# Performance work log

Measured on AMD Instinct MI355X. Metric: run time of the kernel, lower is better.

## Reference

```python
import jax, jax.numpy as jnp
import numpy as np

N_EMBED = 384

def setup_inputs() -> dict:
    key = jax.random.key(0)
    kx, kq, kk, kv = jax.random.split(key, 4)
    B, T, C = 512, 256, N_EMBED
    H = 64
    scale = 1.0 / np.sqrt(C)  # param init scale, keep activations sane
    x = jax.random.normal(kx, (B, T, C), dtype=jnp.float32)
    Wq = jax.random.normal(kq, (C, H), dtype=jnp.float32) * scale
    Wk = jax.random.normal(kk, (C, H), dtype=jnp.float32) * scale
    Wv = jax.random.normal(kv, (C, H), dtype=jnp.float32) * scale
    return {"x": x, "Wq": Wq, "Wk": Wk, "Wv": Wv}

def reference(x, Wq, Wk, Wv):
    B, T, C = x.shape
    q = jnp.einsum('btc,ch->bth', x, Wq)
    k = jnp.einsum('btc,ch->bth', x, Wk)
    v = jnp.einsum('btc,ch->bth', x, Wv)
    # NOTE: original scales by C**-0.5 with C = n_embed (384), not head_size.
    wei = jnp.einsum('bth,bsh->bts', q, k) * (C ** -0.5)  # [B,T,T]
    causal = jnp.tril(jnp.ones((T, T), dtype=bool))
    wei = jnp.where(causal, wei, -jnp.inf)
    wei = jax.nn.softmax(wei, axis=-1)
    out = jnp.einsum('bts,bsh->bth', wei, v)  # [B,T,H]
    return out
```

## Files before the change

kernel.cpp:

```cpp
#include <hip/hip_runtime.h>
#include <hip/hip_bf16.h>


constexpr int BSZ  = 512;
constexpr int TT   = 256;
constexpr int CDIM = 384;
constexpr int HDIM = 64;
constexpr int NQKV = 192;
constexpr float SCALE = 0.051031036307982884f;
constexpr int BTST = 392;

typedef __attribute__((ext_vector_type(8))) short bf16x8;
typedef __attribute__((ext_vector_type(4))) float f32x4;

__device__ inline unsigned short f2bf(float f) {
    __hip_bfloat16 h = __float2bfloat16(f);
    return *(unsigned short*)&h;
}
__device__ inline bf16x8 pack8(float4 a, float4 b) {
    unsigned short p[8] = { f2bf(a.x), f2bf(a.y), f2bf(a.z), f2bf(a.w),
                            f2bf(b.x), f2bf(b.y), f2bf(b.z), f2bf(b.w) };
    return *(bf16x8*)p;
}
__device__ inline unsigned cvtpk(float lo, float hi) {
    unsigned r;
    asm volatile("v_cvt_pk_bf16_f32 %0, %1, %2" : "=v"(r) : "v"(lo), "v"(hi));
    return r;
}
#define PLSWAP32(a, b) asm volatile("v_permlane32_swap_b32 %0, %1" : "+v"(a), "+v"(b))
#define PLSWAP16(a, b) asm volatile("v_permlane16_swap_b32 %0, %1" : "+v"(a), "+v"(b))

__global__ __launch_bounds__(256) void prep_bt(
    const float* __restrict__ Wq, const float* __restrict__ Wk,
    const float* __restrict__ Wv, unsigned short* __restrict__ bt)
{
    int idx = blockIdx.x * 256 + threadIdx.x;
    if (idx >= NQKV * CDIM) return;
    int n = idx / CDIM, k = idx - n * CDIM;
    const float* W = (n < 64) ? Wq : (n < 128) ? Wk : Wv;
    bt[idx] = f2bf(W[(size_t)k * HDIM + (n & 63)]);
}

__global__ __launch_bounds__(1024) void fused(
    const float* __restrict__ x, const unsigned short* __restrict__ bt,
    float* __restrict__ out)
{
    __shared__ __align__(16) unsigned short smem[NQKV * BTST];
    unsigned short* btl = smem;
    unsigned short* qs  = smem;
    unsigned short* kl  = smem + 16384;
    unsigned short* vt  = smem + 32768;

    const int b = blockIdx.x, tid = threadIdx.x;
    const int w = tid >> 6, lane = tid & 63;
    const int lr = lane & 15, lk = lane >> 4;

    const float* xr0 = x + ((size_t)b * TT + 16 * w + lr) * CDIM + lk * 8;

    float4 pA[2], pB[2], pC[2];
#define LDCH(P, ks) { \
    P[0] = *(const float4*)&xr0[(ks) * 32];     \
    P[1] = *(const float4*)&xr0[(ks) * 32 + 4]; }
#define STEP(P, ks, cond) { \
    bf16x8 a = pack8(P[0], P[1]); \
    if (cond) LDCH(P, (ks) + 3); \
    _Pragma("unroll") \
    for (int ni = 0; ni < 12; ++ni) { \
        bf16x8 bb = *(const bf16x8*)&btl[(ni * 16 + lr) * BTST + (ks) * 32 + lk * 8]; \
        acc[ni] = __builtin_amdgcn_mfma_f32_16x16x32_bf16(a, bb, acc[ni], 0, 0, 0); \
    } }

    LDCH(pA, 0) LDCH(pB, 1) LDCH(pC, 2)

    #pragma unroll
    for (int p = 0; p < 9; ++p) {
        int i = p * 1024 + tid;
        int row = i / 48, c8 = i - row * 48;
        *(uint4*)&btl[row * BTST + c8 * 8] = ((const uint4*)bt)[i];
    }
    __syncthreads();

    f32x4 acc[12];
    #pragma unroll
    for (int ni = 0; ni < 12; ++ni) acc[ni] = (f32x4){0.f, 0.f, 0.f, 0.f};

    #pragma unroll
    for (int kk = 0; kk < 4; ++kk) {
        STEP(pA, 3 * kk + 0, kk < 3)
        STEP(pB, 3 * kk + 1, kk < 3)
        STEP(pC, 3 * kk + 2, kk < 3)
    }
#undef LDCH
#undef STEP
    __syncthreads();

    unsigned short* pq = qs + w * 1024;
    #pragma unroll
    for (int ni = 0; ni < 4; ++ni)
        #pragma unroll
        for (int r = 0; r < 4; ++r) {
            int qr = lk * 4 + r;
            int h  = ni * 16 + lr;
            pq[qr * 64 + (h ^ ((qr & 7) << 3))] = f2bf(acc[ni][r] * SCALE);
        }
    #pragma unroll
    for (int ni = 4; ni < 8; ++ni)
        #pragma unroll
        for (int r = 0; r < 4; ++r) {
            int row = 16 * w + lk * 4 + r;
            int c2  = (ni - 4) * 16 + lr;
            kl[row * 64 + (c2 ^ ((row & 7) << 3))] = f2bf(acc[ni][r]);
        }
    #pragma unroll
    for (int ni = 8; ni < 12; ++ni) {
        int h  = (ni - 8) * 16 + lr;
        int t0 = 16 * w + lk * 4;
        unsigned short pk[4];
        #pragma unroll
        for (int r = 0; r < 4; ++r) pk[r] = f2bf(acc[ni][r]);
        *(uint2*)&vt[h * 256 + (t0 ^ ((h & 7) << 3))] = *(uint2*)pk;
    }
    __syncthreads();

    const int q0 = 16 * w;
    bf16x8 qa[2];
    #pragma unroll
    for (int kc = 0; kc < 2; ++kc)
        qa[kc] = *(const bf16x8*)&pq[lr * 64 + ((kc * 32 + lk * 8) ^ ((lr & 7) << 3))];

    f32x4 oacc[4];
    float mrowL = -INFINITY;
    float lpart = 0.f;
    float mrowT[4];
    #pragma unroll
    for (int nh = 0; nh < 4; ++nh) oacc[nh] = (f32x4){0.f, 0.f, 0.f, 0.f};
    #pragma unroll
    for (int r = 0; r < 4; ++r) mrowT[r] = -INFINITY;

    const int lastt = w >> 2;
    for (int st = 0; st <= lastt; ++st) {
        f32x4 sa[4];
        #pragma unroll
        for (int ni = 0; ni < 4; ++ni) sa[ni] = (f32x4){0.f, 0.f, 0.f, 0.f};
        #pragma unroll
        for (int ni = 0; ni < 4; ++ni) {
            int row = st * 64 + ni * 16 + lr;
            #pragma unroll
            for (int kc = 0; kc < 2; ++kc) {
                bf16x8 kb = *(const bf16x8*)
                    &kl[row * 64 + ((kc * 32 + lk * 8) ^ ((row & 7) << 3))];
                sa[ni] = __builtin_amdgcn_mfma_f32_16x16x32_bf16(kb, qa[kc], sa[ni], 0, 0, 0);
            }
        }
        if (st == lastt) {
            #pragma unroll
            for (int ni = 0; ni < 4; ++ni) {
                #pragma unroll
                for (int r = 0; r < 4; ++r) {
                    int sg = st * 64 + ni * 16 + lk * 4 + r;
                    if (sg > q0 + lr) sa[ni][r] = -INFINITY;
                }
            }
        }
        float pm = sa[0][0];
        #pragma unroll
        for (int ni = 0; ni < 4; ++ni)
            #pragma unroll
            for (int r = 0; r < 4; ++r) pm = fmaxf(pm, sa[ni][r]);
        pm = fmaxf(pm, __shfl_xor(pm, 16));
        pm = fmaxf(pm, __shfl_xor(pm, 32));
        float mn = fmaxf(mrowL, pm);
        float corr = __expf(mrowL - mn);
        mrowL = mn;
        lpart *= corr;
        #pragma unroll
        for (int ni = 0; ni < 4; ++ni)
            #pragma unroll
            for (int r = 0; r < 4; ++r) {
                float p = __expf(sa[ni][r] - mn);
                sa[ni][r] = p;
                lpart += p;
            }
        #pragma unroll
        for (int r = 0; r < 4; ++r) {
            float mt = __shfl(mn, lk * 4 + r);
            float ct = __expf(mrowT[r] - mt);
            mrowT[r] = mt;
            #pragma unroll
            for (int nh = 0; nh < 4; ++nh) oacc[nh][r] *= ct;
        }
        unsigned Wp[4][2];
        #pragma unroll
        for (int ni = 0; ni < 4; ++ni) {
            Wp[ni][0] = cvtpk(sa[ni][0], sa[ni][1]);
            Wp[ni][1] = cvtpk(sa[ni][2], sa[ni][3]);
        }
        bf16x8 pa[2];
        #pragma unroll
        for (int kc = 0; kc < 2; ++kc) {
            unsigned x0 = Wp[2 * kc][0], y0 = Wp[2 * kc + 1][0];
            PLSWAP32(x0, y0); PLSWAP16(x0, y0);
            unsigned x1 = Wp[2 * kc][1], y1 = Wp[2 * kc + 1][1];
            PLSWAP32(x1, y1); PLSWAP16(x1, y1);
            unsigned wq[4] = {x0, x1, y0, y1};
            pa[kc] = *(bf16x8*)wq;
        }
        #pragma unroll
        for (int nh = 0; nh < 4; ++nh) {
            int hrow = nh * 16 + lr;
            #pragma unroll
            for (int kc = 0; kc < 2; ++kc) {
                bf16x8 vb = *(const bf16x8*)
                    &vt[hrow * 256 + ((st * 64 + kc * 32 + lk * 8) ^ ((hrow & 7) << 3))];
                oacc[nh] = __builtin_amdgcn_mfma_f32_16x16x32_bf16(pa[kc], vb, oacc[nh], 0, 0, 0);
            }
        }
    }

    float lsum = lpart;
    lsum += __shfl_xor(lsum, 16);
    lsum += __shfl_xor(lsum, 32);
    float linv[4];
    #pragma unroll
    for (int r = 0; r < 4; ++r)
        linv[r] = 1.0f / __shfl(lsum, lk * 4 + r);
    #pragma unroll
    for (int nh = 0; nh < 4; ++nh)
        #pragma unroll
        for (int r = 0; r < 4; ++r) {
            size_t row = (size_t)b * TT + q0 + lk * 4 + r;
            out[row * HDIM + nh * 16 + lr] = oacc[nh][r] * linv[r];
        }
}

extern "C" void kernel_launch(void* const* d_in, const int* in_sizes, int n_in,
                              void* d_out, int out_size, void* d_ws, size_t ws_size,
                              hipStream_t stream)
{
    const float* x  = (const float*)d_in[0];
    const float* Wq = (const float*)d_in[1];
    const float* Wk = (const float*)d_in[2];
    const float* Wv = (const float*)d_in[3];
    unsigned short* bt = (unsigned short*)d_ws;
    float* out = (float*)d_out;

    prep_bt<<<(NQKV * CDIM + 255) / 256, 256, 0, stream>>>(Wq, Wk, Wv, bt);
    fused<<<BSZ, 1024, 0, stream>>>(x, bt, out);
}
```

Before: 61.41 us.

## Retile QKV projection as 32x96 per wave to halve LDS B-fragment reads

The projection GEMM moves from one 16-row by 192-column tile per wave to a 2D layout of 32 rows by 96 columns, so each B fragment loaded from LDS feeds two MFMAs. The prefetch of x is restructured into two double-row register buffers, and the Q/K/V scatter into shared memory is rewritten for the new ownership, with Q now stored globally instead of per wave. Launch bounds now also request a minimum of 4 blocks per CU, which constrains register allocation. The goal is to cut LDS read traffic in the projection phase, at the cost of more live registers for the x prefetch and a branchy store epilogue.

Result: slower. 73.73 us (+20.1%).

```diff
diff --git a/kernel.cpp b/kernel.cpp
--- a/kernel.cpp
+++ b/kernel.cpp
@@ -41,7 +41,7 @@
     bt[idx] = f2bf(W[(size_t)k * HDIM + (n & 63)]);
 }
 
-__global__ __launch_bounds__(1024) void fused(
+__global__ __launch_bounds__(1024, 4) void fused(
     const float* __restrict__ x, const unsigned short* __restrict__ bt,
     float* __restrict__ out)
 {
@@ -55,22 +55,29 @@
     const int w = tid >> 6, lane = tid & 63;
     const int lr = lane & 15, lk = lane >> 4;
 
-    const float* xr0 = x + ((size_t)b * TT + 16 * w + lr) * CDIM + lk * 8;
-
-    float4 pA[2], pB[2], pC[2];
+    const int wr = w >> 1, wc = w & 1;
+    const float* xr0 = x + ((size_t)b * TT + 32 * wr + lr) * CDIM + lk * 8;
+    const float* xr1 = xr0 + 16 * CDIM;
+
+    float4 pA[4], pB[4];
 #define LDCH(P, ks) { \
     P[0] = *(const float4*)&xr0[(ks) * 32];     \
-    P[1] = *(const float4*)&xr0[(ks) * 32 + 4]; }
+    P[1] = *(const float4*)&xr0[(ks) * 32 + 4]; \
+    P[2] = *(const float4*)&xr1[(ks) * 32];     \
+    P[3] = *(const float4*)&xr1[(ks) * 32 + 4]; }
 #define STEP(P, ks, cond) { \
-    bf16x8 a = pack8(P[0], P[1]); \
-    if (cond) LDCH(P, (ks) + 3); \
+    bf16x8 a0 = pack8(P[0], P[1]); \
+    bf16x8 a1 = pack8(P[2], P[3]); \
+    if (cond) LDCH(P, (ks) + 2); \
     _Pragma("unroll") \
-    for (int ni = 0; ni < 12; ++ni) { \
-        bf16x8 bb = *(const bf16x8*)&btl[(ni * 16 + lr) * BTST + (ks) * 32 + lk * 8]; \
-        acc[ni] = __builtin_amdgcn_mfma_f32_16x16x32_bf16(a, bb, acc[ni], 0, 0, 0); \
+    for (int ni = 0; ni < 6; ++ni) { \
+        bf16x8 bb = *(const bf16x8*) \
+            &btl[(96 * wc + ni * 16 + lr) * BTST + (ks) * 32 + lk * 8]; \
+        acc[ni]     = __builtin_amdgcn_mfma_f32_16x16x32_bf16(a0, bb, acc[ni],     0, 0, 0); \
+        acc[6 + ni] = __builtin_amdgcn_mfma_f32_16x16x32_bf16(a1, bb, acc[6 + ni], 0, 0, 0); \
     } }
 
-    LDCH(pA, 0) LDCH(pB, 1) LDCH(pC, 2)
+    LDCH(pA, 0) LDCH(pB, 1)
 
     #pragma unroll
     for (int p = 0; p < 9; ++p) {
@@ -82,43 +89,45 @@
 
     f32x4 acc[12];
     #pragma unroll
-    for (int ni = 0; ni < 12; ++ni) acc[ni] = (f32x4){0.f, 0.f, 0.f, 0.f};
-
-    #pragma unroll
-    for (int kk = 0; kk < 4; ++kk) {
-        STEP(pA, 3 * kk + 0, kk < 3)
-        STEP(pB, 3 * kk + 1, kk < 3)
-        STEP(pC, 3 * kk + 2, kk < 3)
+    for (int i = 0; i < 12; ++i) acc[i] = (f32x4){0.f, 0.f, 0.f, 0.f};
+
+    #pragma unroll
+    for (int kk = 0; kk < 6; ++kk) {
+        STEP(pA, 2 * kk + 0, kk < 5)
+        STEP(pB, 2 * kk + 1, kk < 5)
     }
 #undef LDCH
 #undef STEP
     __syncthreads();
 
-    unsigned short* pq = qs + w * 1024;
-    #pragma unroll
-    for (int ni = 0; ni < 4; ++ni)
-        #pragma unroll
-        for (int r = 0; r < 4; ++r) {
-            int qr = lk * 4 + r;
-            int h  = ni * 16 + lr;
-            pq[qr * 64 + (h ^ ((qr & 7) << 3))] = f2bf(acc[ni][r] * SCALE);
-        }
-    #pragma unroll
-    for (int ni = 4; ni < 8; ++ni)
-        #pragma unroll
-        for (int r = 0; r < 4; ++r) {
-            int row = 16 * w + lk * 4 + r;
-            int c2  = (ni - 4) * 16 + lr;
-            kl[row * 64 + (c2 ^ ((row & 7) << 3))] = f2bf(acc[ni][r]);
-        }
-    #pragma unroll
-    for (int ni = 8; ni < 12; ++ni) {
-        int h  = (ni - 8) * 16 + lr;
-        int t0 = 16 * w + lk * 4;
-        unsigned short pk[4];
-        #pragma unroll
-        for (int r = 0; r < 4; ++r) pk[r] = f2bf(acc[ni][r]);
-        *(uint2*)&vt[h * 256 + (t0 ^ ((h & 7) << 3))] = *(uint2*)pk;
+    #pragma unroll
+    for (int mi = 0; mi < 2; ++mi) {
+        const int rbase = 32 * wr + 16 * mi + lk * 4;
+        #pragma unroll
+        for (int ni = 0; ni < 6; ++ni) {
+            const f32x4 av = acc[mi * 6 + ni];
+            const int col = 96 * wc + ni * 16 + lr;
+            if (col < 64) {
+                #pragma unroll
+                for (int r = 0; r < 4; ++r) {
+                    int row = rbase + r;
+                    qs[row * 64 + (col ^ ((row & 7) << 3))] = f2bf(av[r] * SCALE);
+                }
+            } else if (col < 128) {
+                int c2 = col - 64;
+                #pragma unroll
+                for (int r = 0; r < 4; ++r) {
+                    int row = rbase + r;
+                    kl[row * 64 + (c2 ^ ((row & 7) << 3))] = f2bf(av[r]);
+                }
+            } else {
+                int h = col - 128;
+                unsigned short pk[4];
+                #pragma unroll
+                for (int r = 0; r < 4; ++r) pk[r] = f2bf(av[r]);
+                *(uint2*)&vt[h * 256 + (rbase ^ ((h & 7) << 3))] = *(uint2*)pk;
+            }
+        }
     }
     __syncthreads();
 
@@ -126,7 +135,8 @@
     bf16x8 qa[2];
     #pragma unroll
     for (int kc = 0; kc < 2; ++kc)
-        qa[kc] = *(const bf16x8*)&pq[lr * 64 + ((kc * 32 + lk * 8) ^ ((lr & 7) << 3))];
+        qa[kc] = *(const bf16x8*)
+            &qs[(q0 + lr) * 64 + ((kc * 32 + lk * 8) ^ ((lr & 7) << 3))];
 
     f32x4 oacc[4];
     float mrowL = -INFINITY;
```
